# Kernel tuning notes

Hardware: AMD Instinct MI355X
Metric: run time of the kernel (lower is better)

Reference implementation:

```python
import jax, jax.numpy as jnp
import numpy as np

N = 8192
IN_F = 256
OUT_F = 128
ALPHA = 0.2
NEG = -9000000000000000.0

def setup_inputs() -> dict:
    key = jax.random.key(0)
    k1, k2, k3, k4 = jax.random.split(key, 4)
    h = jax.random.normal(k1, (N, IN_F), dtype=jnp.float32)
    adj = jax.random.randint(k2, (N, N), 0, 2, dtype=jnp.int32)
    # xavier-uniform-like params
    limW = float(np.sqrt(6.0 / (IN_F + OUT_F)))
    W = jax.random.uniform(k3, (IN_F, OUT_F), minval=-limW, maxval=limW, dtype=jnp.float32)
    lima = float(np.sqrt(6.0 / (2 * OUT_F + 1)))
    a = jax.random.uniform(k4, (2 * OUT_F, 1), minval=-lima, maxval=lima, dtype=jnp.float32)
    return {"h": h, "adj": adj, "W": W, "a": a}

def reference(h, adj, W, a):
    Wh = h @ W  # [N, F]
    # e_ij = LeakyReLU(a1.Wh_i + a2.Wh_j) -- avoids [N,N,2F] intermediate
    a1 = a[:OUT_F, 0]  # [F]
    a2 = a[OUT_F:, 0]  # [F]
    f1 = Wh @ a1  # [N]
    f2 = Wh @ a2  # [N]
    e = jax.nn.leaky_relu(f1[:, None] + f2[None, :], negative_slope=ALPHA)  # [N,N]
    att = jnp.where(adj > 0, e, jnp.float32(NEG))
    att = jax.nn.softmax(att, axis=1)
    h_prime = att @ Wh  # [N, F]
    return h_prime
```

## Files before the change

### kernel.cpp

```cpp
#include <hip/hip_runtime.h>
#include <hip/hip_bf16.h>

#define N    8192
#define INF  256
#define OUTF 128
#define ALPHA 0.2f
#define JS   8

typedef __attribute__((ext_vector_type(8))) short bf16x8;
typedef __attribute__((ext_vector_type(4))) float f32x4;

__device__ __forceinline__ unsigned short f2bf(float x) {
    union { float f; unsigned u; } v; v.f = x;
    unsigned r = v.u + 0x7fff + ((v.u >> 16) & 1);
    return (unsigned short)(r >> 16);
}

__global__ __launch_bounds__(256) void k1_wh(
        const float* __restrict__ h, const float* __restrict__ W,
        const float* __restrict__ a,
        unsigned short* __restrict__ WhTb, float* __restrict__ f1, float* __restrict__ f2) {
    __shared__ float hs[8][INF];
    const int t  = threadIdx.x;
    const int i0 = blockIdx.x * 8;

    #pragma unroll
    for (int u = 0; u < 2; ++u) {
        int idx = u * 256 + t;
        int r   = idx >> 6;
        int kq  = idx & 63;
        *(float4*)&hs[r][kq * 4] = *(const float4*)(h + (size_t)(i0 + r) * INF + kq * 4);
    }
    __syncthreads();

    const int rg = t >> 5;
    const int ct = t & 31;
    float acc[4] = {0.f, 0.f, 0.f, 0.f};

    #pragma unroll 8
    for (int k = 0; k < INF; ++k) {
        float4 wv = *(const float4*)(W + (size_t)k * OUTF + ct * 4);
        float  hx = hs[rg][k];
        acc[0] += hx * wv.x; acc[1] += hx * wv.y;
        acc[2] += hx * wv.z; acc[3] += hx * wv.w;
    }

    const int r0 = i0 + rg;
    const int jb = r0 >> 5;
    const int jo = r0 & 31;
    #pragma unroll
    for (int cc = 0; cc < 4; ++cc)
        WhTb[(size_t)jb * 4096 + (ct * 4 + cc) * 32 + jo] = f2bf(acc[cc]);

    const float4 a1v = *(const float4*)(a + ct * 4);
    const float4 a2v = *(const float4*)(a + OUTF + ct * 4);
    float p1 = acc[0]*a1v.x + acc[1]*a1v.y + acc[2]*a1v.z + acc[3]*a1v.w;
    float p2 = acc[0]*a2v.x + acc[1]*a2v.y + acc[2]*a2v.z + acc[3]*a2v.w;
    #pragma unroll
    for (int off = 16; off > 0; off >>= 1) {
        p1 += __shfl_down(p1, off, 32);
        p2 += __shfl_down(p2, off, 32);
    }
    if (ct == 0) { f1[r0] = p1; f2[r0] = p2; }
}

struct PFA { int4 a0, a1; };

__device__ __forceinline__ PFA ldadj(const int* __restrict__ ap, int jt) {
    PFA p;
    p.a0 = *(const int4*)(ap + (size_t)jt * 32);
    p.a1 = *(const int4*)(ap + (size_t)jt * 32 + 4);
    return p;
}

__device__ __forceinline__ float pleak(float f1r, float fv, int av, float& dsum) {
    float s = f1r + fv;
    float e = fmaxf(s, ALPHA * s);
    float p = (av > 0) ? __expf(e) : 0.f;
    dsum += p;
    return p;
}

#define K2STEP(PFV, JT)                                                     \
    {                                                                       \
        const unsigned short* wp_ = WhTb + ((size_t)(tile0 + (JT))) * 4096 + laneb; \
        bf16x8 b0_ = *(const bf16x8*)(wp_);                                 \
        bf16x8 b1_ = *(const bf16x8*)(wp_ + 512);                           \
        bf16x8 b2_ = *(const bf16x8*)(wp_ + 1024);                          \
        bf16x8 b3_ = *(const bf16x8*)(wp_ + 1536);                          \
        bf16x8 b4_ = *(const bf16x8*)(wp_ + 2048);                          \
        bf16x8 b5_ = *(const bf16x8*)(wp_ + 2560);                          \
        bf16x8 b6_ = *(const bf16x8*)(wp_ + 3072);                          \
        bf16x8 b7_ = *(const bf16x8*)(wp_ + 3584);                          \
        float4 F0_ = *(const float4*)(f2p + (size_t)(JT) * 32);             \
        float4 F1_ = *(const float4*)(f2p + (size_t)(JT) * 32 + 4);         \
        int4 A0_ = PFV.a0, A1_ = PFV.a1;                                    \
        if ((JT) + 2 < NT) PFV = ldadj(adjp, (JT) + 2);                     \
        float p0_ = pleak(f1r, F0_.x, A0_.x, dsum);                         \
        float p1_ = pleak(f1r, F0_.y, A0_.y, dsum);                         \
        float p2_ = pleak(f1r, F0_.z, A0_.z, dsum);                         \
        float p3_ = pleak(f1r, F0_.w, A0_.w, dsum);                         \
        float p4_ = pleak(f1r, F1_.x, A1_.x, dsum);                         \
        float p5_ = pleak(f1r, F1_.y, A1_.y, dsum);                         \
        float p6_ = pleak(f1r, F1_.z, A1_.z, dsum);                         \
        float p7_ = pleak(f1r, F1_.w, A1_.w, dsum);                         \
        union { __hip_bfloat162 hh[4]; bf16x8 v; } pk_;                     \
        pk_.hh[0] = __float22bfloat162_rn(make_float2(p0_, p1_));           \
        pk_.hh[1] = __float22bfloat162_rn(make_float2(p2_, p3_));           \
        pk_.hh[2] = __float22bfloat162_rn(make_float2(p4_, p5_));           \
        pk_.hh[3] = __float22bfloat162_rn(make_float2(p6_, p7_));           \
        bf16x8 afrag = pk_.v;                                               \
        acc0 = __builtin_amdgcn_mfma_f32_16x16x32_bf16(afrag, b0_, acc0, 0, 0, 0); \
        acc1 = __builtin_amdgcn_mfma_f32_16x16x32_bf16(afrag, b1_, acc1, 0, 0, 0); \
        acc2 = __builtin_amdgcn_mfma_f32_16x16x32_bf16(afrag, b2_, acc2, 0, 0, 0); \
        acc3 = __builtin_amdgcn_mfma_f32_16x16x32_bf16(afrag, b3_, acc3, 0, 0, 0); \
        acc4 = __builtin_amdgcn_mfma_f32_16x16x32_bf16(afrag, b4_, acc4, 0, 0, 0); \
        acc5 = __builtin_amdgcn_mfma_f32_16x16x32_bf16(afrag, b5_, acc5, 0, 0, 0); \
        acc6 = __builtin_amdgcn_mfma_f32_16x16x32_bf16(afrag, b6_, acc6, 0, 0, 0); \
        acc7 = __builtin_amdgcn_mfma_f32_16x16x32_bf16(afrag, b7_, acc7, 0, 0, 0); \
    }

__global__ __launch_bounds__(256, 4) void k2_attn(
        const int* __restrict__ adj, const unsigned short* __restrict__ WhTb,
        const float* __restrict__ f1, const float* __restrict__ f2,
        float* __restrict__ num, float* __restrict__ den) {
    const int t    = threadIdx.x;
    const int wv   = t >> 6;
    const int ln   = t & 63;
    const int m16  = ln & 15;
    const int quad = ln >> 4;
    const int i0   = blockIdx.x * 64;
    const int s    = blockIdx.y;
    const int row  = i0 + wv * 16 + m16;

    const float f1r  = f1[row];
    const int   j0   = s * (N / JS);
    const int   NT   = (N / JS) / 32;
    const int   tile0 = s * NT;

    const int*   adjp  = adj + (size_t)row * N + j0 + quad * 8;
    const float* f2p   = f2 + j0 + quad * 8;
    const int    laneb = m16 * 32 + quad * 8;

    f32x4 acc0 = {0.f,0.f,0.f,0.f}, acc1 = {0.f,0.f,0.f,0.f};
    f32x4 acc2 = {0.f,0.f,0.f,0.f}, acc3 = {0.f,0.f,0.f,0.f};
    f32x4 acc4 = {0.f,0.f,0.f,0.f}, acc5 = {0.f,0.f,0.f,0.f};
    f32x4 acc6 = {0.f,0.f,0.f,0.f}, acc7 = {0.f,0.f,0.f,0.f};
    float dsum = 0.f;

    PFA pf0 = ldadj(adjp, 0);
    PFA pf1 = ldadj(adjp, 1);

    for (int jt = 0; jt < NT; jt += 2) {
        K2STEP(pf0, jt)
        K2STEP(pf1, jt + 1)
    }

    dsum += __shfl_xor(dsum, 16);
    dsum += __shfl_xor(dsum, 32);
    if (quad == 0) den[(size_t)s * N + row] = dsum;

    float* np = num + (size_t)s * N * OUTF;
    #pragma unroll
    for (int r = 0; r < 4; ++r) {
        const size_t orow = (size_t)(i0 + wv * 16 + quad * 4 + r) * OUTF;
        np[orow + 0 * 16 + m16] = acc0[r];
        np[orow + 1 * 16 + m16] = acc1[r];
        np[orow + 2 * 16 + m16] = acc2[r];
        np[orow + 3 * 16 + m16] = acc3[r];
        np[orow + 4 * 16 + m16] = acc4[r];
        np[orow + 5 * 16 + m16] = acc5[r];
        np[orow + 6 * 16 + m16] = acc6[r];
        np[orow + 7 * 16 + m16] = acc7[r];
    }
}

__global__ __launch_bounds__(256) void k3_combine(
        const float* __restrict__ num, const float* __restrict__ den,
        float* __restrict__ out) {
    const int idx = blockIdx.x * 256 + threadIdx.x;
    const int row = idx >> 5;
    const int c4  = (idx & 31) * 4;
    float4 ns = {0.f,0.f,0.f,0.f};
    float  ds = 0.f;
    #pragma unroll
    for (int s = 0; s < JS; ++s) {
        float4 nv = *(const float4*)(num + ((size_t)s * N + row) * OUTF + c4);
        ns.x += nv.x; ns.y += nv.y; ns.z += nv.z; ns.w += nv.w;
        ds += den[(size_t)s * N + row];
    }
    const float inv = 1.0f / ds;
    float4 o = {ns.x * inv, ns.y * inv, ns.z * inv, ns.w * inv};
    *(float4*)(out + (size_t)row * OUTF + c4) = o;
}

extern "C" void kernel_launch(void* const* d_in, const int* in_sizes, int n_in,
                              void* d_out, int out_size, void* d_ws, size_t ws_size,
                              hipStream_t stream) {
    const float* h   = (const float*)d_in[0];
    const int*   adj = (const int*)  d_in[1];
    const float* W   = (const float*)d_in[2];
    const float* a   = (const float*)d_in[3];
    float* out = (float*)d_out;

    unsigned short* WhTb = (unsigned short*)d_ws;
    float* f1  = (float*)(WhTb + (size_t)N * OUTF);
    float* f2  = f1 + N;
    float* den = f2 + N;
    float* num = den + (size_t)JS * N;

    k1_wh     <<<N / 8, 256, 0, stream>>>(h, W, a, WhTb, f1, f2);
    k2_attn   <<<dim3(N / 64, JS), 256, 0, stream>>>(adj, WhTb, f1, f2, num, den);
    k3_combine<<<(N * OUTF / 4) / 256, 256, 0, stream>>>(num, den, out);
}
```

Measured before the change: 473.8 us.

## Pack adjacency into bitmask and stage Wh tiles through double-buffered LDS

Adds a pre-pass kernel that compresses the int32 adjacency matrix into a bitmask, so the attention kernel reads 32x less mask data per row tile. The attention kernel now stages each bf16 Wh tile in a double-buffered shared-memory buffer shared by all four waves, with f2 cached in LDS. It also doubles the j-split to 16. The 256MB adjacency still has to be read once by the pack kernel. Extra syncthreads per tile and a larger num partial buffer add overhead.

```diff
diff --git a/kernel.cpp b/kernel.cpp
--- a/kernel.cpp
+++ b/kernel.cpp
@@ -5,7 +5,8 @@
 #define INF  256
 #define OUTF 128
 #define ALPHA 0.2f
-#define JS   8
+#define JS   16
+#define NTS  (N / JS / 32)
 
 typedef __attribute__((ext_vector_type(8))) short bf16x8;
 typedef __attribute__((ext_vector_type(4))) float f32x4;
@@ -14,6 +15,22 @@
     union { float f; unsigned u; } v; v.f = x;
     unsigned r = v.u + 0x7fff + ((v.u >> 16) & 1);
     return (unsigned short)(r >> 16);
+}
+
+__global__ __launch_bounds__(256) void k0_pack(
+        const int* __restrict__ adj, unsigned* __restrict__ bits) {
+    const size_t g = (size_t)blockIdx.x * 256 + threadIdx.x;
+    const int4* p = (const int4*)adj + g * 8;
+    unsigned b = 0;
+    #pragma unroll
+    for (int u = 0; u < 8; ++u) {
+        int4 v = p[u];
+        b |= (v.x > 0 ? 1u : 0u) << (u * 4 + 0);
+        b |= (v.y > 0 ? 1u : 0u) << (u * 4 + 1);
+        b |= (v.z > 0 ? 1u : 0u) << (u * 4 + 2);
+        b |= (v.w > 0 ? 1u : 0u) << (u * 4 + 3);
+    }
+    bits[g] = b;
 }
 
 __global__ __launch_bounds__(256) void k1_wh(
@@ -64,52 +81,50 @@
     if (ct == 0) { f1[r0] = p1; f2[r0] = p2; }
 }
 
-struct PFA { int4 a0, a1; };
-
-__device__ __forceinline__ PFA ldadj(const int* __restrict__ ap, int jt) {
-    PFA p;
-    p.a0 = *(const int4*)(ap + (size_t)jt * 32);
-    p.a1 = *(const int4*)(ap + (size_t)jt * 32 + 4);
-    return p;
-}
-
-__device__ __forceinline__ float pleak(float f1r, float fv, int av, float& dsum) {
+__device__ __forceinline__ float pbit(float f1r, float fv, unsigned byte_,
+                                      int u, float& dsum) {
     float s = f1r + fv;
     float e = fmaxf(s, ALPHA * s);
-    float p = (av > 0) ? __expf(e) : 0.f;
+    float p = (byte_ & (1u << u)) ? __expf(e) : 0.f;
     dsum += p;
     return p;
 }
 
-#define K2STEP(PFV, JT)                                                     \
-    {                                                                       \
-        const unsigned short* wp_ = WhTb + ((size_t)(tile0 + (JT))) * 4096 + laneb; \
-        bf16x8 b0_ = *(const bf16x8*)(wp_);                                 \
-        bf16x8 b1_ = *(const bf16x8*)(wp_ + 512);                           \
-        bf16x8 b2_ = *(const bf16x8*)(wp_ + 1024);                          \
-        bf16x8 b3_ = *(const bf16x8*)(wp_ + 1536);                          \
-        bf16x8 b4_ = *(const bf16x8*)(wp_ + 2048);                          \
-        bf16x8 b5_ = *(const bf16x8*)(wp_ + 2560);                          \
-        bf16x8 b6_ = *(const bf16x8*)(wp_ + 3072);                          \
-        bf16x8 b7_ = *(const bf16x8*)(wp_ + 3584);                          \
-        float4 F0_ = *(const float4*)(f2p + (size_t)(JT) * 32);             \
-        float4 F1_ = *(const float4*)(f2p + (size_t)(JT) * 32 + 4);         \
-        int4 A0_ = PFV.a0, A1_ = PFV.a1;                                    \
-        if ((JT) + 2 < NT) PFV = ldadj(adjp, (JT) + 2);                     \
-        float p0_ = pleak(f1r, F0_.x, A0_.x, dsum);                         \
-        float p1_ = pleak(f1r, F0_.y, A0_.y, dsum);                         \
-        float p2_ = pleak(f1r, F0_.z, A0_.z, dsum);                         \
-        float p3_ = pleak(f1r, F0_.w, A0_.w, dsum);                         \
-        float p4_ = pleak(f1r, F1_.x, A1_.x, dsum);                         \
-        float p5_ = pleak(f1r, F1_.y, A1_.y, dsum);                         \
-        float p6_ = pleak(f1r, F1_.z, A1_.z, dsum);                         \
-        float p7_ = pleak(f1r, F1_.w, A1_.w, dsum);                         \
-        union { __hip_bfloat162 hh[4]; bf16x8 v; } pk_;                     \
-        pk_.hh[0] = __float22bfloat162_rn(make_float2(p0_, p1_));           \
-        pk_.hh[1] = __float22bfloat162_rn(make_float2(p2_, p3_));           \
-        pk_.hh[2] = __float22bfloat162_rn(make_float2(p4_, p5_));           \
-        pk_.hh[3] = __float22bfloat162_rn(make_float2(p6_, p7_));           \
-        bf16x8 afrag = pk_.v;                                               \
+#define K2SUB(WORD, JT)                                                      \
+    {                                                                        \
+        const int cb_ = (JT) & 1, nb_ = ((JT) + 1) & 1;                      \
+        float4 sg0_, sg1_;                                                   \
+        if ((JT) + 1 < NTS) {                                                \
+            const char* ws_ = (const char*)WhTb + (size_t)(tile0 + (JT) + 1) * 8192; \
+            sg0_ = *(const float4*)(ws_ + t * 16);                           \
+            sg1_ = *(const float4*)(ws_ + 4096 + t * 16);                    \
+        }                                                                    \
+        float4 F0_ = *(const float4*)&f2s[(JT) * 32 + quad * 8];             \
+        float4 F1_ = *(const float4*)&f2s[(JT) * 32 + quad * 8 + 4];         \
+        unsigned byte_ = ((WORD) >> (quad << 3)) & 0xffu;                    \
+        float p0_ = pbit(f1r, F0_.x, byte_, 0, dsum);                        \
+        float p1_ = pbit(f1r, F0_.y, byte_, 1, dsum);                        \
+        float p2_ = pbit(f1r, F0_.z, byte_, 2, dsum);                        \
+        float p3_ = pbit(f1r, F0_.w, byte_, 3, dsum);                        \
+        float p4_ = pbit(f1r, F1_.x, byte_, 4, dsum);                        \
+        float p5_ = pbit(f1r, F1_.y, byte_, 5, dsum);                        \
+        float p6_ = pbit(f1r, F1_.z, byte_, 6, dsum);                        \
+        float p7_ = pbit(f1r, F1_.w, byte_, 7, dsum);                        \
+        union { __hip_bfloat162 hh[4]; bf16x8 v; } pk_;                      \
+        pk_.hh[0] = __float22bfloat162_rn(make_float2(p0_, p1_));            \
+        pk_.hh[1] = __float22bfloat162_rn(make_float2(p2_, p3_));            \
+        pk_.hh[2] = __float22bfloat162_rn(make_float2(p4_, p5_));            \
+        pk_.hh[3] = __float22bfloat162_rn(make_float2(p6_, p7_));            \
+        bf16x8 afrag = pk_.v;                                                \
+        const char* bb_ = (const char*)&bsm[cb_][0] + laneb2;                \
+        bf16x8 b0_ = *(const bf16x8*)(bb_);                                  \
+        bf16x8 b1_ = *(const bf16x8*)(bb_ + 1024);                           \
+        bf16x8 b2_ = *(const bf16x8*)(bb_ + 2048);                           \
+        bf16x8 b3_ = *(const bf16x8*)(bb_ + 3072);                           \
+        bf16x8 b4_ = *(const bf16x8*)(bb_ + 4096);                           \
+        bf16x8 b5_ = *(const bf16x8*)(bb_ + 5120);                           \
+        bf16x8 b6_ = *(const bf16x8*)(bb_ + 6144);                           \
+        bf16x8 b7_ = *(const bf16x8*)(bb_ + 7168);                           \
         acc0 = __builtin_amdgcn_mfma_f32_16x16x32_bf16(afrag, b0_, acc0, 0, 0, 0); \
         acc1 = __builtin_amdgcn_mfma_f32_16x16x32_bf16(afrag, b1_, acc1, 0, 0, 0); \
         acc2 = __builtin_amdgcn_mfma_f32_16x16x32_bf16(afrag, b2_, acc2, 0, 0, 0); \
@@ -118,12 +133,21 @@
         acc5 = __builtin_amdgcn_mfma_f32_16x16x32_bf16(afrag, b5_, acc5, 0, 0, 0); \
         acc6 = __builtin_amdgcn_mfma_f32_16x16x32_bf16(afrag, b6_, acc6, 0, 0, 0); \
         acc7 = __builtin_amdgcn_mfma_f32_16x16x32_bf16(afrag, b7_, acc7, 0, 0, 0); \
-    }
-
-__global__ __launch_bounds__(256, 4) void k2_attn(
-        const int* __restrict__ adj, const unsigned short* __restrict__ WhTb,
+        if ((JT) + 1 < NTS) {                                                \
+            char* bd_ = (char*)&bsm[nb_][0];                                 \
+            *(float4*)(bd_ + t * 16)        = sg0_;                          \
+            *(float4*)(bd_ + 4096 + t * 16) = sg1_;                          \
+        }                                                                    \
+        __syncthreads();                                                     \
+    }
+
+__global__ __launch_bounds__(256, 5) void k2_attn(
+        const unsigned* __restrict__ bits, const unsigned short* __restrict__ WhTb,
         const float* __restrict__ f1, const float* __restrict__ f2,
         float* __restrict__ num, float* __restrict__ den) {
+    __shared__ unsigned short bsm[2][4096];
+    __shared__ float f2s[512];
+
     const int t    = threadIdx.x;
     const int wv   = t >> 6;
     const int ln   = t & 63;
@@ -132,15 +156,23 @@
     const int i0   = blockIdx.x * 64;
     const int s    = blockIdx.y;
     const int row  = i0 + wv * 16 + m16;
-
-    const float f1r  = f1[row];
-    const int   j0   = s * (N / JS);
-    const int   NT   = (N / JS) / 32;
-    const int   tile0 = s * NT;
-
-    const int*   adjp  = adj + (size_t)row * N + j0 + quad * 8;
-    const float* f2p   = f2 + j0 + quad * 8;
-    const int    laneb = m16 * 32 + quad * 8;
+    const int tile0 = s * NTS;
+    const int j0    = s * (N / JS);
+    const int laneb2 = (m16 * 32 + quad * 8) * 2;
+
+    if (t < 128) *(float4*)&f2s[t * 4] = *(const float4*)(f2 + j0 + t * 4);
+    {
+        const char* ws0 = (const char*)WhTb + (size_t)tile0 * 8192;
+        float4 s0 = *(const float4*)(ws0 + t * 16);
+        float4 s1 = *(const float4*)(ws0 + 4096 + t * 16);
+        char* bd = (char*)&bsm[0][0];
+        *(float4*)(bd + t * 16)        = s0;
+        *(float4*)(bd + 4096 + t * 16) = s1;
+    }
+
+    const float f1r = f1[row];
+    const uint4* brow = (const uint4*)((const char*)bits + (size_t)row * 1024 + (size_t)tile0 * 4);
+    uint4 bw0 = brow[0], bw1 = brow[1], bw2 = brow[2], bw3 = brow[3];
 
     f32x4 acc0 = {0.f,0.f,0.f,0.f}, acc1 = {0.f,0.f,0.f,0.f};
     f32x4 acc2 = {0.f,0.f,0.f,0.f}, acc3 = {0.f,0.f,0.f,0.f};
@@ -148,13 +180,12 @@
     f32x4 acc6 = {0.f,0.f,0.f,0.f}, acc7 = {0.f,0.f,0.f,0.f};
     float dsum = 0.f;
 
-    PFA pf0 = ldadj(adjp, 0);
-    PFA pf1 = ldadj(adjp, 1);
-
-    for (int jt = 0; jt < NT; jt += 2) {
-        K2STEP(pf0, jt)
-        K2STEP(pf1, jt + 1)
-    }
+    __syncthreads();
+
+    K2SUB(bw0.x,  0) K2SUB(bw0.y,  1) K2SUB(bw0.z,  2) K2SUB(bw0.w,  3)
+    K2SUB(bw1.x,  4) K2SUB(bw1.y,  5) K2SUB(bw1.z,  6) K2SUB(bw1.w,  7)
+    K2SUB(bw2.x,  8) K2SUB(bw2.y,  9) K2SUB(bw2.z, 10) K2SUB(bw2.w, 11)
+    K2SUB(bw3.x, 12) K2SUB(bw3.y, 13) K2SUB(bw3.z, 14) K2SUB(bw3.w, 15)
 
     dsum += __shfl_xor(dsum, 16);
     dsum += __shfl_xor(dsum, 32);
@@ -204,12 +235,14 @@
     float* out = (float*)d_out;
 
     unsigned short* WhTb = (unsigned short*)d_ws;
-    float* f1  = (float*)(WhTb + (size_t)N * OUTF);
-    float* f2  = f1 + N;
-    float* den = f2 + N;
-    float* num = den + (size_t)JS * N;
+    float*    f1   = (float*)(WhTb + (size_t)N * OUTF);
+    float*    f2   = f1 + N;
+    float*    den  = f2 + N;
+    unsigned* bits = (unsigned*)(den + (size_t)JS * N);
+    float*    num  = (float*)(bits + (size_t)N * (N / 32));
 
     k1_wh     <<<N / 8, 256, 0, stream>>>(h, W, a, WhTb, f1, f2);
-    k2_attn   <<<dim3(N / 64, JS), 256, 0, stream>>>(adj, WhTb, f1, f2, num, den);
+    k0_pack   <<<(N / 32) * (N / 256), 256, 0, stream>>>(adj, bits);
+    k2_attn   <<<dim3(N / 64, JS), 256, 0, stream>>>(bits, WhTb, f1, f2, num, den);
     k3_combine<<<(N * OUTF / 4) / 256, 256, 0, stream>>>(num, den, out);
 }
```

Result: faster. 452.8 us (-4.4%).
